# Performance work log

Measured on AMD Instinct MI355X. Metric: run time of the kernel, lower is better.

## Reference

```python
import jax, jax.numpy as jnp
import numpy as np

BS, S, D, H, HS, HSEL, L = 32, 512, 512, 8, 2, 4, 6
DK = D // H  # 64
HD = H - HS  # dynamic heads


def setup_inputs() -> dict:
    key = jax.random.key(0)
    ks = jax.random.split(key, 10)
    w = lambda k, shape: jax.random.normal(k, shape, dtype=jnp.float32) * 0.02
    return {
        'q_embed_data': jax.random.normal(ks[0], (BS, S, D), jnp.float32),
        'qa_embed_data': jax.random.normal(ks[1], (BS, S, D), jnp.float32),
        # stacked per-layer params (torch Linear convention: W[out,in], y = x@W.T+b)
        'Wq': w(ks[2], (L, D, D)), 'bq': jnp.zeros((L, D), jnp.float32),
        'Wv': w(ks[3], (L, D, D)), 'bv': jnp.zeros((L, D), jnp.float32),
        'Wg': w(ks[4], (L, HD, D)),                      # routing gate, no bias
        'Wo': w(ks[5], (L, D, D)), 'bo': jnp.zeros((L, D), jnp.float32),
        'ln1_g': jnp.ones((L, D), jnp.float32), 'ln1_b': jnp.zeros((L, D), jnp.float32),
        'W1': w(ks[6], (L, D, D)), 'b1': jnp.zeros((L, D), jnp.float32),
        'W2': w(ks[7], (L, D, D)), 'b2': jnp.zeros((L, D), jnp.float32),
        'ln2_g': jnp.ones((L, D), jnp.float32), 'ln2_b': jnp.zeros((L, D), jnp.float32),
    }


def _layer_norm(x, g, b):
    m = x.mean(-1, keepdims=True)
    v = ((x - m) ** 2).mean(-1, keepdims=True)
    return (x - m) * jax.lax.rsqrt(v + 1e-5) * g + b


def _moh_attention(xq, xv, Wq, bq, Wv, bv, Wg, Wo, bo, strict):
    bs, s, d = xq.shape
    q = xq @ Wq.T + bq            # kq_same=True: k = q projection
    v = xv @ Wv.T + bv
    qh = q.reshape(bs, s, H, DK).transpose(0, 2, 1, 3)   # [b,h,s,dk]
    vh = v.reshape(bs, s, H, DK).transpose(0, 2, 1, 3)
    scores = jnp.einsum('bhqd,bhkd->bhqk', qh, qh) / jnp.sqrt(jnp.float32(DK))
    # mask==1 -> causal incl. diag; mask==0 -> strictly causal
    allow = jnp.tril(jnp.ones((s, s), bool), k=-1 if strict else 0)
    scores = jnp.where(allow, scores, jnp.float32(-1e9))
    # pad-zero shift: first query row replaced by zeros -> uniform attention
    scores = scores.at[:, :, 0, :].set(0.0)
    # per-token top-k head routing over dynamic heads
    gates = jax.nn.softmax(q.reshape(bs * s, D) @ Wg.T, axis=-1)  # [bs*s, HD]
    _, idx = jax.lax.top_k(gates, HSEL)
    dmask = jnp.zeros_like(gates).at[jnp.arange(bs * s)[:, None], idx].set(1.0)
    dyn = (gates * dmask).reshape(bs, s, HD)
    routing = jnp.concatenate([jnp.ones((bs, s, HS), gates.dtype), dyn], -1).mean(1)  # [b,H]
    attn = jax.nn.softmax(scores, axis=-1)
    ctx = jnp.einsum('bhqk,bhkd->bhqd', attn, vh) * routing[:, :, None, None]
    out = ctx.transpose(0, 2, 1, 3).reshape(bs, s, D) @ Wo.T + bo
    f = dmask.sum(0)
    P = gates.mean(0)
    balance = jnp.sum((f / (f.sum() + 1e-5)) * (P / (P.sum() + 1e-5)))
    return out, balance


def reference(q_embed_data, qa_embed_data, Wq, bq, Wv, bv, Wg, Wo, bo,
              ln1_g, ln1_b, W1, b1, W2, b2, ln2_g, ln2_b):
    def layer(i, xq, xv, strict):
        a, bl = _moh_attention(xq, xv, Wq[i], bq[i], Wv[i], bv[i], Wg[i], Wo[i], bo[i], strict)
        x = _layer_norm(xq + a, ln1_g[i], ln1_b[i])
        ffn = jax.nn.relu(x @ W1[i].T + b1[i]) @ W2[i].T + b2[i]
        return _layer_norm(x + ffn, ln2_g[i], ln2_b[i]), bl

    y = qa_embed_data
    x = q_embed_data
    # blocks_1: self-attention on y, mask=1
    y, _ = layer(0, y, y, False)
    y, _ = layer(1, y, y, False)
    # blocks_2: alternate mask=1 self-attn / mask=0 cross-attn (values=y)
    x, _ = layer(2, x, x, False)
    x, bl = layer(3, x, y, True)
    x, _ = layer(4, x, x, False)
    x, bl = layer(5, x, y, True)
    return (x, bl)
```

## Files before the change

kernel.cpp:

```cpp
#include <hip/hip_runtime.h>
#include <cstdint>

#define BSZ 32
#define SEQ 512
#define DM  512
#define NH  8
#define DK  64
#define HS_ 2
#define HD_ 6
#define NL  6
#define MROWS (BSZ*SEQ)
#define QVLD 1024
#define SCL 0.18033688011112043f

typedef unsigned short bf16_t;
typedef __attribute__((ext_vector_type(4))) float f32x4;
typedef __attribute__((ext_vector_type(8))) short bf16x8;
typedef __attribute__((ext_vector_type(8))) unsigned short u16x8;

#define DEV static __device__ __forceinline__

DEV float bf2f(bf16_t b) {
  unsigned int u = ((unsigned int)b) << 16;
  float f; __builtin_memcpy(&f, &u, 4); return f;
}
DEV bf16_t f2b(float f) {
  unsigned int u; __builtin_memcpy(&u, &f, 4);
  unsigned int r = (u + 0x7fffu + ((u >> 16) & 1u)) >> 16;
  return (bf16_t)r;
}
DEV void unp2(unsigned int w, float& a, float& b) {
  unsigned int ua = w << 16, ub = w & 0xffff0000u;
  __builtin_memcpy(&a, &ua, 4); __builtin_memcpy(&b, &ub, 4);
}
DEV unsigned cvtpk(float lo, float hi) {
  unsigned r;
  asm("v_cvt_pk_bf16_f32 %0, %1, %2" : "=v"(r) : "v"(lo), "v"(hi));
  return r;
}

DEV void gload_lds16(const bf16_t* g, bf16_t* l) {
  __builtin_amdgcn_global_load_lds(
      (const __attribute__((address_space(1))) void*)g,
      (__attribute__((address_space(3))) void*)l, 16, 0, 0);
}

DEV bf16x8 scale_q(bf16x8 v) {
  u16x8 u;
  __builtin_memcpy(&u, &v, 16);
  unsigned w[4];
#pragma unroll
  for (int e = 0; e < 4; ++e)
    w[e] = cvtpk(bf2f(u[2 * e]) * SCL, bf2f(u[2 * e + 1]) * SCL);
  bf16x8 r;
  __builtin_memcpy(&r, w, 16);
  return r;
}

__global__ __launch_bounds__(256) void f2b2_kernel(
    const float* __restrict__ s0, const float* __restrict__ s1,
    bf16_t* __restrict__ d0, bf16_t* __restrict__ d1) {
  const float* s = blockIdx.y ? s1 : s0;
  bf16_t* d = blockIdx.y ? d1 : d0;
  const int i = blockIdx.x * 256 + threadIdx.x;
  float4 v = reinterpret_cast<const float4*>(s)[i];
  ushort4 o;
  o.x = f2b(v.x); o.y = f2b(v.y); o.z = f2b(v.z); o.w = f2b(v.w);
  reinterpret_cast<ushort4*>(d)[i] = o;
}

__global__ __launch_bounds__(256) void f2bw_kernel(
    const float* __restrict__ s0, const float* __restrict__ s1,
    const float* __restrict__ s2, const float* __restrict__ s3,
    const float* __restrict__ s4, bf16_t* __restrict__ dst) {
  const float* srcs[5] = {s0, s1, s2, s3, s4};
  const float* s = srcs[blockIdx.y];
  bf16_t* d = dst + (size_t)blockIdx.y * ((size_t)NL * DM * DM);
  const int i = blockIdx.x * 256 + threadIdx.x;
  float4 v = reinterpret_cast<const float4*>(s)[i];
  ushort4 o;
  o.x = f2b(v.x); o.y = f2b(v.y); o.z = f2b(v.z); o.w = f2b(v.w);
  reinterpret_cast<ushort4*>(d)[i] = o;
}

template <int NB, int NWG, bool RELU>
__global__ __launch_bounds__(512) void gemm8(
    const bf16_t* __restrict__ A0, const bf16_t* __restrict__ A1,
    const bf16_t* __restrict__ W0, const bf16_t* __restrict__ W1,
    const float* __restrict__ b0, const float* __restrict__ b1,
    bf16_t* __restrict__ Yb, int ldy) {
  const int K = 512;
  const int lin = blockIdx.y * NB + blockIdx.x;
  const int cpx = NWG / 8;
  const int swz = (lin & 7) * cpx + (lin >> 3);
  const int bn = swz % NB, bm = swz / NB;
  const int tid = threadIdx.x, wid = tid >> 6, lane = tid & 63;
  const int wr = wid >> 2, wc = wid & 3;
  const int lrow = lane & 15, grp = lane >> 4;
  const int l3 = lane >> 3, c3 = lane & 7;

  __shared__ __align__(16) bf16_t Lds[3][24576];

  const bool hi = (bn * 256) >= 512;
  const bf16_t* Asel = hi ? A1 : A0;
  const bf16_t* Wsel = hi ? (W1 - (size_t)512 * K) : W0;
  const float* bsel = hi ? (b1 - 512) : b0;

  f32x4 acc[4][4];
#pragma unroll
  for (int m = 0; m < 4; ++m)
#pragma unroll
    for (int n = 0; n < 4; ++n) acc[m][n] = f32x4{0.f, 0.f, 0.f, 0.f};

  const char* LB = (const char*)Lds;

  auto stage3 = [&](int kt, int buf, int half) {
#pragma unroll
    for (int cc = 0; cc < 3; ++cc) {
      const int c = wid + (half * 3 + cc) * 8;
      const int colb = ((c3 ^ l3) * 8);
      if (c < 16) {
        gload_lds16(Asel + (size_t)(bm * 128 + c * 8 + l3) * K + kt * 64 + colb,
                    &Lds[buf][c * 512]);
      } else {
        const int cb = c - 16;
        gload_lds16(Wsel + (size_t)(bn * 256 + cb * 8 + l3) * K + kt * 64 + colb,
                    &Lds[buf][8192 + cb * 512]);
      }
    }
  };
  auto rdA = [&](int buf, int rA, int ks) -> bf16x8 {
    const int off = buf * 49152 + rA * 128 + ((ks * 64 + grp * 16) ^ ((rA & 7) << 4));
    return *reinterpret_cast<const bf16x8*>(LB + off);
  };
  auto rdB = [&](int buf, int rB, int ks) -> bf16x8 {
    const int off = buf * 49152 + 16384 + rB * 128 + ((ks * 64 + grp * 16) ^ ((rB & 7) << 4));
    return *reinterpret_cast<const bf16x8*>(LB + off);
  };

  stage3(0, 0, 0); stage3(0, 0, 1);
  stage3(1, 1, 0); stage3(1, 1, 1);
  asm volatile("s_waitcnt vmcnt(6)" ::: "memory");
  __builtin_amdgcn_s_barrier();

  for (int g = 0; g < 8; ++g) {
    const int bufR = g % 3, bufW = (g + 2) % 3;
    const bool st = g < 6;
    bf16x8 bwv[4][2], afv[2][2];
#pragma unroll
    for (int n = 0; n < 4; ++n)
#pragma unroll
      for (int ks = 0; ks < 2; ++ks)
        bwv[n][ks] = rdB(bufR, wc * 64 + n * 16 + lrow, ks);
#pragma unroll
    for (int m = 0; m < 2; ++m)
#pragma unroll
      for (int ks = 0; ks < 2; ++ks)
        afv[m][ks] = rdA(bufR, wr * 64 + m * 16 + lrow, ks);
    if (st) stage3(g + 2, bufW, 0);
    __builtin_amdgcn_s_barrier();
    asm volatile("s_waitcnt lgkmcnt(0)" ::: "memory");
    __builtin_amdgcn_s_setprio(1);
#pragma unroll
    for (int ks = 0; ks < 2; ++ks)
#pragma unroll
      for (int m = 0; m < 2; ++m)
#pragma unroll
        for (int n = 0; n < 4; ++n)
          acc[m][n] = __builtin_amdgcn_mfma_f32_16x16x32_bf16(afv[m][ks], bwv[n][ks], acc[m][n], 0, 0, 0);
    __builtin_amdgcn_s_setprio(0);
    __builtin_amdgcn_s_barrier();
#pragma unroll
    for (int m = 0; m < 2; ++m)
#pragma unroll
      for (int ks = 0; ks < 2; ++ks)
        afv[m][ks] = rdA(bufR, wr * 64 + 32 + m * 16 + lrow, ks);
    if (st) stage3(g + 2, bufW, 1);
    __builtin_amdgcn_s_barrier();
    asm volatile("s_waitcnt lgkmcnt(0)" ::: "memory");
    __builtin_amdgcn_s_setprio(1);
#pragma unroll
    for (int ks = 0; ks < 2; ++ks)
#pragma unroll
      for (int m = 0; m < 2; ++m)
#pragma unroll
        for (int n = 0; n < 4; ++n)
          acc[2 + m][n] = __builtin_amdgcn_mfma_f32_16x16x32_bf16(afv[m][ks], bwv[n][ks], acc[2 + m][n], 0, 0, 0);
    __builtin_amdgcn_s_setprio(0);
    if (g < 6) {
      asm volatile("s_waitcnt vmcnt(6)" ::: "memory");
    } else if (g == 6) {
      asm volatile("s_waitcnt vmcnt(0)" ::: "memory");
    }
    __builtin_amdgcn_s_barrier();
  }

  const int r0 = bm * 128 + wr * 64 + grp * 4;
  const int c0 = bn * 256 + wc * 64 + lrow;
#pragma unroll
  for (int n = 0; n < 4; ++n) {
    const int col = c0 + n * 16;
    const float bc = bsel[col];
#pragma unroll
    for (int qm = 0; qm < 4; ++qm)
#pragma unroll
      for (int j = 0; j < 4; ++j) {
        float v = acc[qm][n][j] + bc;
        if (RELU) v = fmaxf(v, 0.f);
        Yb[(size_t)(r0 + qm * 16 + j) * ldy + col] = f2b(v);
      }
  }
}

template <int OUT>
__global__ __launch_bounds__(512) void gemm_ln(
    const bf16_t* __restrict__ A, const bf16_t* __restrict__ W,
    const float* __restrict__ bias, const bf16_t* __restrict__ Res,
    const float* __restrict__ gam, const float* __restrict__ bet,
    bf16_t* __restrict__ outb, float* __restrict__ outf) {
  const int K = 512;
  const int bm = blockIdx.x;
  const int tid = threadIdx.x, wid = tid >> 6, lane = tid & 63;
  const int lrow = lane & 15, grp = lane >> 4;
  const int l3 = lane >> 3, c3 = lane & 7;

  __shared__ __align__(16) bf16_t Lds[2][36864];
  __shared__ float red_s[64][8], red_q[64][8], stat[64][2];

  f32x4 acc[4][4];
#pragma unroll
  for (int m = 0; m < 4; ++m)
#pragma unroll
    for (int n = 0; n < 4; ++n) acc[m][n] = f32x4{0.f, 0.f, 0.f, 0.f};

  const char* LB = (const char*)Lds;

  auto stage = [&](int kt, int buf) {
#pragma unroll
    for (int k = 0; k < 9; ++k) {
      const int c = wid + k * 8;
      const int colb = (c3 ^ l3) * 8;
      if (c < 8) {
        gload_lds16(A + (size_t)(bm * 64 + c * 8 + l3) * K + kt * 64 + colb,
                    &Lds[buf][c * 512]);
      } else {
        const int cb = c - 8;
        gload_lds16(W + (size_t)(cb * 8 + l3) * K + kt * 64 + colb,
                    &Lds[buf][4096 + cb * 512]);
      }
    }
  };
  auto rdA = [&](int buf, int r, int ks) -> bf16x8 {
    const int off = buf * 73728 + r * 128 + ((ks * 64 + grp * 16) ^ ((r & 7) << 4));
    return *reinterpret_cast<const bf16x8*>(LB + off);
  };
  auto rdW = [&](int buf, int r, int ks) -> bf16x8 {
    const int off = buf * 73728 + 8192 + r * 128 + ((ks * 64 + grp * 16) ^ ((r & 7) << 4));
    return *reinterpret_cast<const bf16x8*>(LB + off);
  };

  stage(0, 0);
  __syncthreads();
  for (int g = 0; g < 8; ++g) {
    const int bufR = g & 1;
    if (g < 7) stage(g + 1, bufR ^ 1);
    bf16x8 af[4][2], wf[4][2];
#pragma unroll
    for (int m = 0; m < 4; ++m)
#pragma unroll
      for (int ks = 0; ks < 2; ++ks)
        af[m][ks] = rdA(bufR, m * 16 + lrow, ks);
#pragma unroll
    for (int n = 0; n < 4; ++n)
#pragma unroll
      for (int ks = 0; ks < 2; ++ks)
        wf[n][ks] = rdW(bufR, wid * 64 + n * 16 + lrow, ks);
    __builtin_amdgcn_s_setprio(1);
#pragma unroll
    for (int ks = 0; ks < 2; ++ks)
#pragma unroll
      for (int m = 0; m < 4; ++m)
#pragma unroll
        for (int n = 0; n < 4; ++n)
          acc[m][n] = __builtin_amdgcn_mfma_f32_16x16x32_bf16(af[m][ks], wf[n][ks], acc[m][n], 0, 0, 0);
    __builtin_amdgcn_s_setprio(0);
    __syncthreads();
  }

  const int cbase = wid * 64;
  float bias_n[4], gam_n[4], bet_n[4];
#pragma unroll
  for (int n = 0; n < 4; ++n) {
    bias_n[n] = bias[cbase + n * 16 + lrow];
    gam_n[n]  = gam[cbase + n * 16 + lrow];
    bet_n[n]  = bet[cbase + n * 16 + lrow];
  }
  const size_t rowg0 = (size_t)bm * 64;
  float ps[4][4], pq[4][4];
#pragma unroll
  for (int m = 0; m < 4; ++m)
#pragma unroll
    for (int j = 0; j < 4; ++j) {
      const int r = m * 16 + grp * 4 + j;
      float s = 0.f, q = 0.f;
#pragma unroll
      for (int n = 0; n < 4; ++n) {
        float z = acc[m][n][j] + bias_n[n] +
                  bf2f(Res[(rowg0 + r) * DM + cbase + n * 16 + lrow]);
        acc[m][n][j] = z;
        s += z; q += z * z;
      }
      ps[m][j] = s; pq[m][j] = q;
    }
#pragma unroll
  for (int m = 0; m < 4; ++m)
#pragma unroll
    for (int j = 0; j < 4; ++j)
#pragma unroll
      for (int off = 1; off <= 8; off <<= 1) {
        ps[m][j] += __shfl_xor(ps[m][j], off);
        pq[m][j] += __shfl_xor(pq[m][j], off);
      }
  if (lrow == 0) {
#pragma unroll
    for (int m = 0; m < 4; ++m)
#pragma unroll
      for (int j = 0; j < 4; ++j) {
        const int r = m * 16 + grp * 4 + j;
        red_s[r][wid] = ps[m][j];
        red_q[r][wid] = pq[m][j];
      }
  }
  __syncthreads();
  if (tid < 64) {
    float s = 0.f, q = 0.f;
#pragma unroll
    for (int w = 0; w < 8; ++w) { s += red_s[tid][w]; q += red_q[tid][w]; }
    const float mean = s * (1.f / 512.f);
    const float var = q * (1.f / 512.f) - mean * mean;
    stat[tid][0] = mean;
    stat[tid][1] = rsqrtf(var + 1e-5f);
  }
  __syncthreads();
#pragma unroll
  for (int m = 0; m < 4; ++m)
#pragma unroll
    for (int j = 0; j < 4; ++j) {
      const int r = m * 16 + grp * 4 + j;
      const float mean = stat[r][0], rstd = stat[r][1];
#pragma unroll
      for (int n = 0; n < 4; ++n) {
        const float o = (acc[m][n][j] - mean) * rstd * gam_n[n] + bet_n[n];
        const size_t off = (rowg0 + r) * DM + cbase + n * 16 + lrow;
        if (OUT == 0) outb[off] = f2b(o);
        else outf[off] = o;
      }
    }
}

__global__ __launch_bounds__(256) void gates_kernel(
    const bf16_t* __restrict__ qv, const float* __restrict__ Wg,
    float* __restrict__ rdyn, float* __restrict__ fP) {
  __shared__ float wg_s[HD_ * DM];
  __shared__ float blk[4][18];
  const int tid = threadIdx.x, wid = tid >> 6, lane = tid & 63;
  for (int i = tid; i < HD_ * DM / 4; i += 256)
    reinterpret_cast<float4*>(wg_s)[i] = reinterpret_cast<const float4*>(Wg)[i];
  __syncthreads();
  const int bb = blockIdx.x >> 4;
  const int t0 = (blockIdx.x & 15) * 32 + wid * 8;
  float fs[6] = {0, 0, 0, 0, 0, 0}, ps[6] = {0, 0, 0, 0, 0, 0}, rs[6] = {0, 0, 0, 0, 0, 0};
  for (int it = 0; it < 8; ++it) {
    const int tok = bb * SEQ + t0 + it;
    uint4 u = reinterpret_cast<const uint4*>(qv + (size_t)tok * QVLD)[lane];
    float x[8];
    unp2(u.x, x[0], x[1]); unp2(u.y, x[2], x[3]);
    unp2(u.z, x[4], x[5]); unp2(u.w, x[6], x[7]);
    float g[6];
#pragma unroll
    for (int j = 0; j < 6; ++j) {
      float p = 0.f;
#pragma unroll
      for (int e = 0; e < 8; ++e) p = fmaf(x[e], wg_s[j * DM + lane * 8 + e], p);
#pragma unroll
      for (int off = 32; off; off >>= 1) p += __shfl_xor(p, off);
      g[j] = p;
    }
    float mx = g[0];
#pragma unroll
    for (int j = 1; j < 6; ++j) mx = fmaxf(mx, g[j]);
    float se = 0.f;
#pragma unroll
    for (int j = 0; j < 6; ++j) { g[j] = __expf(g[j] - mx); se += g[j]; }
    float inv = 1.f / se;
#pragma unroll
    for (int j = 0; j < 6; ++j) g[j] *= inv;
    int d1 = 0;
#pragma unroll
    for (int j = 1; j < 6; ++j)
      if (g[j] < g[d1] || (g[j] == g[d1] && j > d1)) d1 = j;
    int d2 = (d1 == 0) ? 1 : 0;
#pragma unroll
    for (int j = 0; j < 6; ++j) {
      if (j == d1) continue;
      if (g[j] < g[d2] || (g[j] == g[d2] && j > d2)) d2 = j;
    }
#pragma unroll
    for (int j = 0; j < 6; ++j) {
      const bool drop = (j == d1) || (j == d2);
      fs[j] += drop ? 0.f : 1.f;
      ps[j] += g[j];
      rs[j] += drop ? 0.f : g[j];
    }
  }
  if (lane == 0) {
#pragma unroll
    for (int j = 0; j < 6; ++j) {
      blk[wid][j] = fs[j]; blk[wid][6 + j] = ps[j]; blk[wid][12 + j] = rs[j];
    }
  }
  __syncthreads();
  if (tid < 18) {
    float s = blk[0][tid] + blk[1][tid] + blk[2][tid] + blk[3][tid];
    if (tid < 12) atomicAdd(&fP[tid], s);
    else atomicAdd(&rdyn[bb * 6 + (tid - 12)], s * (1.f / 512.f));
  }
}

__global__ __launch_bounds__(256, 4) void fattn_kernel(
    const bf16_t* __restrict__ qv, const float* __restrict__ rdyn,
    bf16_t* __restrict__ ctx, int strict) {
  const int bh = blockIdx.x, qt = blockIdx.y;
  const int b = bh >> 3, h = bh & 7;
  const int tid = threadIdx.x, wid = tid >> 6, lane = tid & 63;
  const int c0 = lane & 15, grp = lane >> 4;
  const int l3 = lane >> 3, c3 = lane & 7;
  const int kidx = lane & 31, dhalf = lane >> 5;

  __shared__ __align__(16) bf16_t Ks[64 * 64];
  __shared__ __align__(16) bf16_t Vt[64 * 72];
  __shared__ __align__(16) bf16_t Ps[4][32 * 64];
  __shared__ float csum[64];

  const bf16_t* qp = qv;
  const bf16_t* vp = qv + 512;
  const float factor = (h < HS_) ? 1.f : rdyn[b * 6 + (h - HS_)];

  const int qbase = qt * 128 + wid * 32;

  bf16x8 qf[2][2];
#pragma unroll
  for (int nt = 0; nt < 2; ++nt)
#pragma unroll
    for (int ks = 0; ks < 2; ++ks)
      qf[nt][ks] = scale_q(*reinterpret_cast<const bf16x8*>(
          qp + ((size_t)(b * SEQ + qbase + nt * 16 + c0)) * QVLD + h * DK + ks * 32 + grp * 8));

  f32x4 acc[2][4];
#pragma unroll
  for (int m = 0; m < 2; ++m)
#pragma unroll
    for (int d = 0; d < 4; ++d) acc[m][d] = f32x4{0.f, 0.f, 0.f, 0.f};
  float mreg[2] = {-3e38f, -3e38f};
  float lreg[2] = {0.f, 0.f};
  float cs[8] = {0, 0, 0, 0, 0, 0, 0, 0};

  const int lastk = (qbase + 31 - strict) >> 6;
  const int ktmax = 2 * qt + 1;

  for (int kt = 0; kt <= ktmax; ++kt) {
#pragma unroll
    for (int i = 0; i < 2; ++i) {
      int row = i * 32 + wid * 8 + l3;
      int blk = c3 ^ l3;
      gload_lds16(qp + ((size_t)(b * SEQ + kt * 64 + row)) * QVLD + h * DK + blk * 8,
                  Ks + (i * 32 + wid * 8) * 64);
    }
#pragma unroll
    for (int j = 0; j < 2; ++j) {
      const int d0 = (wid * 2 + j) * 8 + dhalf * 4;
      const bf16_t* src = vp + ((size_t)(b * SEQ + kt * 64 + 2 * kidx)) * QVLD + h * DK + d0;
      ushort4 lo = *reinterpret_cast<const ushort4*>(src);
      ushort4 hv = *reinterpret_cast<const ushort4*>(src + QVLD);
      *reinterpret_cast<unsigned*>(&Vt[(d0 + 0) * 72 + 2 * kidx]) = (unsigned)lo.x | ((unsigned)hv.x << 16);
      *reinterpret_cast<unsigned*>(&Vt[(d0 + 1) * 72 + 2 * kidx]) = (unsigned)lo.y | ((unsigned)hv.y << 16);
      *reinterpret_cast<unsigned*>(&Vt[(d0 + 2) * 72 + 2 * kidx]) = (unsigned)lo.z | ((unsigned)hv.z << 16);
      *reinterpret_cast<unsigned*>(&Vt[(d0 + 3) * 72 + 2 * kidx]) = (unsigned)lo.w | ((unsigned)hv.w << 16);
      if (qt == 3) {
        cs[j * 4 + 0] += bf2f(lo.x) + bf2f(hv.x);
        cs[j * 4 + 1] += bf2f(lo.y) + bf2f(hv.y);
        cs[j * 4 + 2] += bf2f(lo.z) + bf2f(hv.z);
        cs[j * 4 + 3] += bf2f(lo.w) + bf2f(hv.w);
      }
    }
    __syncthreads();

    if (kt <= lastk) {
      const char* KsB = (const char*)Ks;
      bf16x8 kf[4][2];
#pragma unroll
      for (int mt = 0; mt < 4; ++mt)
#pragma unroll
        for (int ks = 0; ks < 2; ++ks)
          kf[mt][ks] = *reinterpret_cast<const bf16x8*>(
              KsB + (mt * 16 + c0) * 128 + 16 * ((4 * ks + grp) ^ (c0 & 7)));
      f32x4 s[4][2];
#pragma unroll
      for (int mt = 0; mt < 4; ++mt)
#pragma unroll
        for (int nt = 0; nt < 2; ++nt) s[mt][nt] = f32x4{0.f, 0.f, 0.f, 0.f};
      __builtin_amdgcn_s_setprio(1);
#pragma unroll
      for (int mt = 0; mt < 4; ++mt)
#pragma unroll
        for (int nt = 0; nt < 2; ++nt)
#pragma unroll
          for (int ks = 0; ks < 2; ++ks)
            s[mt][nt] = __builtin_amdgcn_mfma_f32_16x16x32_bf16(
                kf[mt][ks], qf[nt][ks], s[mt][nt], 0, 0, 0);
      __builtin_amdgcn_s_setprio(0);

      const bool masked = (kt == lastk);
      if (masked) {
#pragma unroll
        for (int nt = 0; nt < 2; ++nt) {
          const int q = qbase + nt * 16 + c0;
#pragma unroll
          for (int mt = 0; mt < 4; ++mt)
#pragma unroll
            for (int j = 0; j < 4; ++j) {
              int k = kt * 64 + mt * 16 + grp * 4 + j;
              if (k + strict > q) s[mt][nt][j] = -1e30f;
            }
        }
      }
      float mx[2];
#pragma unroll
      for (int nt = 0; nt < 2; ++nt) {
        float a = fmaxf(s[0][nt][0], s[0][nt][1]);
        a = fmaxf(fmaxf(a, s[0][nt][2]), s[0][nt][3]);
        float bm_ = fmaxf(s[1][nt][0], s[1][nt][1]);
        bm_ = fmaxf(fmaxf(bm_, s[1][nt][2]), s[1][nt][3]);
        float c = fmaxf(s[2][nt][0], s[2][nt][1]);
        c = fmaxf(fmaxf(c, s[2][nt][2]), s[2][nt][3]);
        float d = fmaxf(s[3][nt][0], s[3][nt][1]);
        d = fmaxf(fmaxf(d, s[3][nt][2]), s[3][nt][3]);
        float m_ = fmaxf(fmaxf(a, bm_), fmaxf(c, d));
        m_ = fmaxf(m_, __shfl_xor(m_, 16));
        m_ = fmaxf(m_, __shfl_xor(m_, 32));
        mx[nt] = m_;
      }
      const bool defer = __all((mx[0] - mreg[0] <= 8.f) && (mx[1] - mreg[1] <= 8.f));
      float sc[2];
#pragma unroll
      for (int nt = 0; nt < 2; ++nt) {
        const float mnew = defer ? mreg[nt] : fmaxf(mreg[nt], mx[nt]);
        float ts = 0.f;
#pragma unroll
        for (int mt = 0; mt < 4; ++mt)
#pragma unroll
          for (int j = 0; j < 4; ++j) {
            float pp = exp2f(s[mt][nt][j] - mnew);
            s[mt][nt][j] = pp; ts += pp;
          }
        ts += __shfl_xor(ts, 16);
        ts += __shfl_xor(ts, 32);
        if (defer) {
          lreg[nt] += ts;
        } else {
          sc[nt] = exp2f(mreg[nt] - mnew);
          lreg[nt] = lreg[nt] * sc[nt] + ts;
          mreg[nt] = mnew;
        }
      }
      char* PsB = (char*)(&Ps[wid][0]);
#pragma unroll
      for (int nt = 0; nt < 2; ++nt)
#pragma unroll
        for (int mt = 0; mt < 4; ++mt) {
          uint2 w;
          w.x = cvtpk(s[mt][nt][0], s[mt][nt][1]);
          w.y = cvtpk(s[mt][nt][2], s[mt][nt][3]);
          int row = nt * 16 + c0;
          int off = (row * 128 + mt * 32 + grp * 8) ^ ((c0 & 7) << 4);
          *reinterpret_cast<uint2*>(PsB + off) = w;
        }
      if (!defer) {
#pragma unroll
        for (int mtq = 0; mtq < 2; ++mtq) {
          f32x4 sv;
#pragma unroll
          for (int j = 0; j < 4; ++j) sv[j] = __shfl(sc[mtq], grp * 4 + j);
#pragma unroll
          for (int dt = 0; dt < 4; ++dt) acc[mtq][dt] *= sv;
        }
      }
      bf16x8 pf[2][2], vf2[4][2];
#pragma unroll
      for (int mtq = 0; mtq < 2; ++mtq)
#pragma unroll
        for (int ks = 0; ks < 2; ++ks)
          pf[mtq][ks] = *reinterpret_cast<const bf16x8*>(
              PsB + (mtq * 16 + c0) * 128 + 16 * ((4 * ks + grp) ^ (c0 & 7)));
#pragma unroll
      for (int dt = 0; dt < 4; ++dt)
#pragma unroll
        for (int ks = 0; ks < 2; ++ks)
          vf2[dt][ks] = *reinterpret_cast<const bf16x8*>(
              (const char*)Vt + (dt * 16 + c0) * 144 + ks * 64 + grp * 16);
      __builtin_amdgcn_s_setprio(1);
#pragma unroll
      for (int mtq = 0; mtq < 2; ++mtq)
#pragma unroll
        for (int dt = 0; dt < 4; ++dt)
#pragma unroll
          for (int ks = 0; ks < 2; ++ks)
            acc[mtq][dt] = __builtin_amdgcn_mfma_f32_16x16x32_bf16(
                pf[mtq][ks], vf2[dt][ks], acc[mtq][dt], 0, 0, 0);
      __builtin_amdgcn_s_setprio(0);
    }
    __syncthreads();
  }

  if (qt == 3) {
#pragma unroll
    for (int e = 0; e < 8; ++e)
#pragma unroll
      for (int off = 1; off <= 16; off <<= 1) cs[e] += __shfl_xor(cs[e], off);
    if ((lane & 31) == 0) {
#pragma unroll
      for (int e = 0; e < 8; ++e)
        csum[(wid * 2 + (e >> 2)) * 8 + dhalf * 4 + (e & 3)] = cs[e];
    }
    __syncthreads();
    if (tid < 64)
      ctx[((size_t)(b * SEQ)) * DM + h * DK + tid] = f2b(csum[tid] * (1.f / 512.f) * factor);
  }

#pragma unroll
  for (int mtq = 0; mtq < 2; ++mtq) {
    const float inv = factor / lreg[mtq];
    f32x4 iv;
#pragma unroll
    for (int j = 0; j < 4; ++j) iv[j] = __shfl(inv, grp * 4 + j);
#pragma unroll
    for (int j = 0; j < 4; ++j) {
      const int q = qbase + mtq * 16 + grp * 4 + j;
      if (q == 0) continue;
#pragma unroll
      for (int dt = 0; dt < 4; ++dt)
        ctx[((size_t)(b * SEQ + q)) * DM + h * DK + dt * 16 + c0] =
            f2b(acc[mtq][dt][j] * iv[j]);
    }
  }
}

__global__ void balance_kernel(const float* __restrict__ fP, float* __restrict__ out) {
  if (threadIdx.x == 0 && blockIdx.x == 0) {
    float fs = 0.f, pssum = 0.f, P[6];
    for (int j = 0; j < 6; ++j) {
      fs += fP[j];
      P[j] = fP[6 + j] * (1.f / (float)MROWS);
      pssum += P[j];
    }
    float bal = 0.f;
    for (int j = 0; j < 6; ++j)
      bal += (fP[j] / (fs + 1e-5f)) * (P[j] / (pssum + 1e-5f));
    out[0] = bal;
  }
}

extern "C" void kernel_launch(void* const* d_in, const int* in_sizes, int n_in,
                              void* d_out, int out_size, void* d_ws, size_t ws_size,
                              hipStream_t stream) {
  (void)in_sizes; (void)n_in; (void)out_size; (void)ws_size;
  const float* q_embed  = (const float*)d_in[0];
  const float* qa_embed = (const float*)d_in[1];
  const float* Wq  = (const float*)d_in[2];
  const float* bq  = (const float*)d_in[3];
  const float* Wv  = (const float*)d_in[4];
  const float* bv  = (const float*)d_in[5];
  const float* Wg  = (const float*)d_in[6];
  const float* Wo  = (const float*)d_in[7];
  const float* bo  = (const float*)d_in[8];
  const float* ln1g = (const float*)d_in[9];
  const float* ln1b = (const float*)d_in[10];
  const float* W1  = (const float*)d_in[11];
  const float* b1  = (const float*)d_in[12];
  const float* W2  = (const float*)d_in[13];
  const float* b2  = (const float*)d_in[14];
  const float* ln2g = (const float*)d_in[15];
  const float* ln2b = (const float*)d_in[16];

  char* p = (char*)d_ws;
  auto alloc = [&](size_t bytes) -> char* {
    char* r = p; p += (bytes + 255) & ~(size_t)255; return r;
  };
  const size_t WDE = (size_t)NL * DM * DM;
  const size_t AE  = (size_t)MROWS * DM;
  bf16_t* wall_b = (bf16_t*)alloc(5 * WDE * 2);
  bf16_t* wq_b = wall_b;
  bf16_t* wv_b = wall_b + WDE;
  bf16_t* wo_b = wall_b + 2 * WDE;
  bf16_t* w1_b = wall_b + 3 * WDE;
  bf16_t* w2_b = wall_b + 4 * WDE;
  bf16_t* y_b   = (bf16_t*)alloc(AE * 2);
  bf16_t* x_b   = (bf16_t*)alloc(AE * 2);
  bf16_t* qv_b  = (bf16_t*)alloc((size_t)MROWS * QVLD * 2);
  bf16_t* ctx_b = (bf16_t*)alloc(AE * 2);
  bf16_t* x1_b  = (bf16_t*)alloc(AE * 2);
  bf16_t* ffn1_b = (bf16_t*)alloc(AE * 2);
  float* stats = (float*)alloc(NL * (12 + BSZ * 6) * 4);
  float* fPbase = stats;
  float* rdynbase = stats + NL * 12;

  hipMemsetAsync(stats, 0, NL * (12 + BSZ * 6) * 4, stream);

  f2bw_kernel<<<dim3((unsigned)(WDE / 4 / 256), 5), 256, 0, stream>>>(
      Wq, Wv, Wo, W1, W2, wall_b);
  f2b2_kernel<<<dim3((unsigned)(AE / 4 / 256), 2), 256, 0, stream>>>(
      qa_embed, q_embed, y_b, x_b);

  const size_t DD = (size_t)DM * DM;
  dim3 gqv(4, 128), gn5(2, 128), gfa(256, 4), gln(256);
  float* outx = (float*)d_out;

  auto layer = [&](int i, bf16_t* resb, const bf16_t* xvb, int strict, bool last) {
    float* fP = fPbase + i * 12;
    float* rdyn = rdynbase + i * (BSZ * 6);
    gemm8<4, 512, false><<<gqv, 512, 0, stream>>>(
        resb, xvb, wq_b + i * DD, wv_b + i * DD, bq + i * DM, bv + i * DM, qv_b, QVLD);
    gates_kernel<<<MROWS / 32, 256, 0, stream>>>(qv_b, Wg + (size_t)i * HD_ * DM, rdyn, fP);
    fattn_kernel<<<gfa, 256, 0, stream>>>(qv_b, rdyn, ctx_b, strict);
    gemm_ln<0><<<gln, 512, 0, stream>>>(
        ctx_b, wo_b + i * DD, bo + i * DM, resb, ln1g + i * DM, ln1b + i * DM,
        x1_b, nullptr);
    gemm8<2, 256, true><<<gn5, 512, 0, stream>>>(
        x1_b, x1_b, w1_b + i * DD, w1_b + i * DD, b1 + i * DM, b1 + i * DM, ffn1_b, DM);
    if (last)
      gemm_ln<1><<<gln, 512, 0, stream>>>(
          ffn1_b, w2_b + i * DD, b2 + i * DM, x1_b, ln2g + i * DM, ln2b + i * DM,
          nullptr, outx);
    else
      gemm_ln<0><<<gln, 512, 0, stream>>>(
          ffn1_b, w2_b + i * DD, b2 + i * DM, x1_b, ln2g + i * DM, ln2b + i * DM,
          resb, nullptr);
  };

  layer(0, y_b, y_b, 0, false);
  layer(1, y_b, y_b, 0, false);
  layer(2, x_b, x_b, 0, false);
  layer(3, x_b, y_b, 1, false);
  layer(4, x_b, x_b, 0, false);
  layer(5, x_b, y_b, 1, true);
  balance_kernel<<<1, 64, 0, stream>>>(fPbase + 5 * 12, outx + (size_t)MROWS * DM);
}
```

Before: 951.5 us.

## Batch independent layers 0 and 2 into shared grid launches

Layers 0 (on y) and 2 (on x) do not depend on each other, so they now run together: each kernel takes two argument structs and uses a grid z or y dimension to pick one. This doubles the grid size for that unit and removes six kernel launches, aiming to fill the GPU better and overlap the two independent chains. Separate qv, ctx, x1 and ffn1 buffers are allocated for the second stream. The fattn launch bound also changes from 4 to 2 blocks per SM, which relaxes register pressure but may lower occupancy.

```diff
diff --git a/kernel.cpp b/kernel.cpp
--- a/kernel.cpp
+++ b/kernel.cpp
@@ -56,6 +56,12 @@
   __builtin_memcpy(&r, w, 16);
   return r;
 }
+
+struct G8A { const bf16_t *A0, *A1, *W0, *W1; const float *b0, *b1; bf16_t* Y; };
+struct GLA { const bf16_t *A, *W; const float* bias; const bf16_t* Res;
+             const float *gam, *bet; bf16_t* outb; float* outf; };
+struct FAA { const bf16_t* qv; const float* rdyn; bf16_t* ctx; };
+struct GTA { const bf16_t* qv; const float* Wg; float* rdyn; float* fP; };
 
 __global__ __launch_bounds__(256) void f2b2_kernel(
     const float* __restrict__ s0, const float* __restrict__ s1,
@@ -84,11 +90,8 @@
 }
 
 template <int NB, int NWG, bool RELU>
-__global__ __launch_bounds__(512) void gemm8(
-    const bf16_t* __restrict__ A0, const bf16_t* __restrict__ A1,
-    const bf16_t* __restrict__ W0, const bf16_t* __restrict__ W1,
-    const float* __restrict__ b0, const float* __restrict__ b1,
-    bf16_t* __restrict__ Yb, int ldy) {
+__global__ __launch_bounds__(512) void gemm8(G8A ia, G8A ib, int ldy) {
+  const G8A& P = blockIdx.z ? ib : ia;
   const int K = 512;
   const int lin = blockIdx.y * NB + blockIdx.x;
   const int cpx = NWG / 8;
@@ -102,9 +105,9 @@
   __shared__ __align__(16) bf16_t Lds[3][24576];
 
   const bool hi = (bn * 256) >= 512;
-  const bf16_t* Asel = hi ? A1 : A0;
-  const bf16_t* Wsel = hi ? (W1 - (size_t)512 * K) : W0;
-  const float* bsel = hi ? (b1 - 512) : b0;
+  const bf16_t* Asel = hi ? P.A1 : P.A0;
+  const bf16_t* Wsel = hi ? (P.W1 - (size_t)512 * K) : P.W0;
+  const float* bsel = hi ? (P.b1 - 512) : P.b0;
 
   f32x4 acc[4][4];
 #pragma unroll
@@ -207,17 +210,14 @@
       for (int j = 0; j < 4; ++j) {
         float v = acc[qm][n][j] + bc;
         if (RELU) v = fmaxf(v, 0.f);
-        Yb[(size_t)(r0 + qm * 16 + j) * ldy + col] = f2b(v);
+        P.Y[(size_t)(r0 + qm * 16 + j) * ldy + col] = f2b(v);
       }
   }
 }
 
 template <int OUT>
-__global__ __launch_bounds__(512) void gemm_ln(
-    const bf16_t* __restrict__ A, const bf16_t* __restrict__ W,
-    const float* __restrict__ bias, const bf16_t* __restrict__ Res,
-    const float* __restrict__ gam, const float* __restrict__ bet,
-    bf16_t* __restrict__ outb, float* __restrict__ outf) {
+__global__ __launch_bounds__(512) void gemm_ln(GLA ia, GLA ib) {
+  const GLA& P = blockIdx.y ? ib : ia;
   const int K = 512;
   const int bm = blockIdx.x;
   const int tid = threadIdx.x, wid = tid >> 6, lane = tid & 63;
@@ -241,11 +241,11 @@
       const int c = wid + k * 8;
       const int colb = (c3 ^ l3) * 8;
       if (c < 8) {
-        gload_lds16(A + (size_t)(bm * 64 + c * 8 + l3) * K + kt * 64 + colb,
+        gload_lds16(P.A + (size_t)(bm * 64 + c * 8 + l3) * K + kt * 64 + colb,
                     &Lds[buf][c * 512]);
       } else {
         const int cb = c - 8;
-        gload_lds16(W + (size_t)(cb * 8 + l3) * K + kt * 64 + colb,
+        gload_lds16(P.W + (size_t)(cb * 8 + l3) * K + kt * 64 + colb,
                     &Lds[buf][4096 + cb * 512]);
       }
     }
@@ -291,9 +291,9 @@
   float bias_n[4], gam_n[4], bet_n[4];
 #pragma unroll
   for (int n = 0; n < 4; ++n) {
-    bias_n[n] = bias[cbase + n * 16 + lrow];
-    gam_n[n]  = gam[cbase + n * 16 + lrow];
-    bet_n[n]  = bet[cbase + n * 16 + lrow];
+    bias_n[n] = P.bias[cbase + n * 16 + lrow];
+    gam_n[n]  = P.gam[cbase + n * 16 + lrow];
+    bet_n[n]  = P.bet[cbase + n * 16 + lrow];
   }
   const size_t rowg0 = (size_t)bm * 64;
   float ps[4][4], pq[4][4];
@@ -306,7 +306,7 @@
 #pragma unroll
       for (int n = 0; n < 4; ++n) {
         float z = acc[m][n][j] + bias_n[n] +
-                  bf2f(Res[(rowg0 + r) * DM + cbase + n * 16 + lrow]);
+                  bf2f(P.Res[(rowg0 + r) * DM + cbase + n * 16 + lrow]);
         acc[m][n][j] = z;
         s += z; q += z * z;
       }
@@ -352,27 +352,26 @@
       for (int n = 0; n < 4; ++n) {
         const float o = (acc[m][n][j] - mean) * rstd * gam_n[n] + bet_n[n];
         const size_t off = (rowg0 + r) * DM + cbase + n * 16 + lrow;
-        if (OUT == 0) outb[off] = f2b(o);
-        else outf[off] = o;
-      }
-    }
-}
-
-__global__ __launch_bounds__(256) void gates_kernel(
-    const bf16_t* __restrict__ qv, const float* __restrict__ Wg,
-    float* __restrict__ rdyn, float* __restrict__ fP) {
+        if (OUT == 0) P.outb[off] = f2b(o);
+        else P.outf[off] = o;
+      }
+    }
+}
+
+__global__ __launch_bounds__(256) void gates_kernel(GTA ia, GTA ib) {
+  const GTA& P = blockIdx.y ? ib : ia;
   __shared__ float wg_s[HD_ * DM];
   __shared__ float blk[4][18];
   const int tid = threadIdx.x, wid = tid >> 6, lane = tid & 63;
   for (int i = tid; i < HD_ * DM / 4; i += 256)
-    reinterpret_cast<float4*>(wg_s)[i] = reinterpret_cast<const float4*>(Wg)[i];
+    reinterpret_cast<float4*>(wg_s)[i] = reinterpret_cast<const float4*>(P.Wg)[i];
   __syncthreads();
   const int bb = blockIdx.x >> 4;
   const int t0 = (blockIdx.x & 15) * 32 + wid * 8;
   float fs[6] = {0, 0, 0, 0, 0, 0}, ps[6] = {0, 0, 0, 0, 0, 0}, rs[6] = {0, 0, 0, 0, 0, 0};
   for (int it = 0; it < 8; ++it) {
     const int tok = bb * SEQ + t0 + it;
-    uint4 u = reinterpret_cast<const uint4*>(qv + (size_t)tok * QVLD)[lane];
+    uint4 u = reinterpret_cast<const uint4*>(P.qv + (size_t)tok * QVLD)[lane];
     float x[8];
     unp2(u.x, x[0], x[1]); unp2(u.y, x[2], x[3]);
     unp2(u.z, x[4], x[5]); unp2(u.w, x[6], x[7]);
@@ -422,14 +421,13 @@
   __syncthreads();
   if (tid < 18) {
     float s = blk[0][tid] + blk[1][tid] + blk[2][tid] + blk[3][tid];
-    if (tid < 12) atomicAdd(&fP[tid], s);
-    else atomicAdd(&rdyn[bb * 6 + (tid - 12)], s * (1.f / 512.f));
-  }
-}
-
-__global__ __launch_bounds__(256, 4) void fattn_kernel(
-    const bf16_t* __restrict__ qv, const float* __restrict__ rdyn,
-    bf16_t* __restrict__ ctx, int strict) {
+    if (tid < 12) atomicAdd(&P.fP[tid], s);
+    else atomicAdd(&P.rdyn[bb * 6 + (tid - 12)], s * (1.f / 512.f));
+  }
+}
+
+__global__ __launch_bounds__(256, 2) void fattn_kernel(FAA ia, FAA ib, int strict) {
+  const FAA& P = blockIdx.z ? ib : ia;
   const int bh = blockIdx.x, qt = blockIdx.y;
   const int b = bh >> 3, h = bh & 7;
   const int tid = threadIdx.x, wid = tid >> 6, lane = tid & 63;
@@ -442,9 +440,9 @@
   __shared__ __align__(16) bf16_t Ps[4][32 * 64];
   __shared__ float csum[64];
 
-  const bf16_t* qp = qv;
-  const bf16_t* vp = qv + 512;
-  const float factor = (h < HS_) ? 1.f : rdyn[b * 6 + (h - HS_)];
+  const bf16_t* qp = P.qv;
+  const bf16_t* vp = P.qv + 512;
+  const float factor = (h < HS_) ? 1.f : P.rdyn[b * 6 + (h - HS_)];
 
   const int qbase = qt * 128 + wid * 32;
 
@@ -634,7 +632,7 @@
     }
     __syncthreads();
     if (tid < 64)
-      ctx[((size_t)(b * SEQ)) * DM + h * DK + tid] = f2b(csum[tid] * (1.f / 512.f) * factor);
+      P.ctx[((size_t)(b * SEQ)) * DM + h * DK + tid] = f2b(csum[tid] * (1.f / 512.f) * factor);
   }
 
 #pragma unroll
@@ -649,7 +647,7 @@
       if (q == 0) continue;
 #pragma unroll
       for (int dt = 0; dt < 4; ++dt)
-        ctx[((size_t)(b * SEQ + q)) * DM + h * DK + dt * 16 + c0] =
+        P.ctx[((size_t)(b * SEQ + q)) * DM + h * DK + dt * 16 + c0] =
             f2b(acc[mtq][dt][j] * iv[j]);
     }
   }
@@ -707,9 +705,13 @@
   bf16_t* y_b   = (bf16_t*)alloc(AE * 2);
   bf16_t* x_b   = (bf16_t*)alloc(AE * 2);
   bf16_t* qv_b  = (bf16_t*)alloc((size_t)MROWS * QVLD * 2);
-  bf16_t* ctx_b = (bf16_t*)alloc(AE * 2);
-  bf16_t* x1_b  = (bf16_t*)alloc(AE * 2);
-  bf16_t* ffn1_b = (bf16_t*)alloc(AE * 2);
+  bf16_t* qv2_b = (bf16_t*)alloc((size_t)MROWS * QVLD * 2);
+  bf16_t* ctx_b  = (bf16_t*)alloc(AE * 2);
+  bf16_t* ctx2_b = (bf16_t*)alloc(AE * 2);
+  bf16_t* x1_b   = (bf16_t*)alloc(AE * 2);
+  bf16_t* x12_b  = (bf16_t*)alloc(AE * 2);
+  bf16_t* ffn1_b  = (bf16_t*)alloc(AE * 2);
+  bf16_t* ffn12_b = (bf16_t*)alloc(AE * 2);
   float* stats = (float*)alloc(NL * (12 + BSZ * 6) * 4);
   float* fPbase = stats;
   float* rdynbase = stats + NL * 12;
@@ -722,36 +724,48 @@
       qa_embed, q_embed, y_b, x_b);
 
   const size_t DD = (size_t)DM * DM;
-  dim3 gqv(4, 128), gn5(2, 128), gfa(256, 4), gln(256);
   float* outx = (float*)d_out;
 
-  auto layer = [&](int i, bf16_t* resb, const bf16_t* xvb, int strict, bool last) {
-    float* fP = fPbase + i * 12;
-    float* rdyn = rdynbase + i * (BSZ * 6);
-    gemm8<4, 512, false><<<gqv, 512, 0, stream>>>(
-        resb, xvb, wq_b + i * DD, wv_b + i * DD, bq + i * DM, bv + i * DM, qv_b, QVLD);
-    gates_kernel<<<MROWS / 32, 256, 0, stream>>>(qv_b, Wg + (size_t)i * HD_ * DM, rdyn, fP);
-    fattn_kernel<<<gfa, 256, 0, stream>>>(qv_b, rdyn, ctx_b, strict);
-    gemm_ln<0><<<gln, 512, 0, stream>>>(
-        ctx_b, wo_b + i * DD, bo + i * DM, resb, ln1g + i * DM, ln1b + i * DM,
-        x1_b, nullptr);
-    gemm8<2, 256, true><<<gn5, 512, 0, stream>>>(
-        x1_b, x1_b, w1_b + i * DD, w1_b + i * DD, b1 + i * DM, b1 + i * DM, ffn1_b, DM);
-    if (last)
-      gemm_ln<1><<<gln, 512, 0, stream>>>(
-          ffn1_b, w2_b + i * DD, b2 + i * DM, x1_b, ln2g + i * DM, ln2b + i * DM,
-          nullptr, outx);
-    else
-      gemm_ln<0><<<gln, 512, 0, stream>>>(
-          ffn1_b, w2_b + i * DD, b2 + i * DM, x1_b, ln2g + i * DM, ln2b + i * DM,
-          resb, nullptr);
+  struct Bufs { bf16_t *qv, *ctx, *x1, *ffn1; };
+  Bufs B0{qv_b, ctx_b, x1_b, ffn1_b}, B1{qv2_b, ctx2_b, x12_b, ffn12_b};
+
+  auto unit = [&](int nb, int i0, int i1, bf16_t* res0, const bf16_t* xv0,
+                  bf16_t* res1, const bf16_t* xv1, int strict, bool last) {
+    G8A qa{res0, xv0, wq_b + i0 * DD, wv_b + i0 * DD, bq + i0 * DM, bv + i0 * DM, B0.qv};
+    G8A qb{res1, xv1, wq_b + i1 * DD, wv_b + i1 * DD, bq + i1 * DM, bv + i1 * DM, B1.qv};
+    gemm8<4, 512, false><<<dim3(4, 128, nb), 512, 0, stream>>>(qa, qb, QVLD);
+
+    GTA ga{B0.qv, Wg + (size_t)i0 * HD_ * DM, rdynbase + i0 * (BSZ * 6), fPbase + i0 * 12};
+    GTA gb{B1.qv, Wg + (size_t)i1 * HD_ * DM, rdynbase + i1 * (BSZ * 6), fPbase + i1 * 12};
+    gates_kernel<<<dim3(MROWS / 32, nb), 256, 0, stream>>>(ga, gb);
+
+    FAA fa{B0.qv, rdynbase + i0 * (BSZ * 6), B0.ctx};
+    FAA fb{B1.qv, rdynbase + i1 * (BSZ * 6), B1.ctx};
+    fattn_kernel<<<dim3(256, 4, nb), 256, 0, stream>>>(fa, fb, strict);
+
+    GLA la{B0.ctx, wo_b + i0 * DD, bo + i0 * DM, res0, ln1g + i0 * DM, ln1b + i0 * DM, B0.x1, nullptr};
+    GLA lb{B1.ctx, wo_b + i1 * DD, bo + i1 * DM, res1, ln1g + i1 * DM, ln1b + i1 * DM, B1.x1, nullptr};
+    gemm_ln<0><<<dim3(256, nb), 512, 0, stream>>>(la, lb);
+
+    G8A f1a{B0.x1, B0.x1, w1_b + i0 * DD, w1_b + i0 * DD, b1 + i0 * DM, b1 + i0 * DM, B0.ffn1};
+    G8A f1b{B1.x1, B1.x1, w1_b + i1 * DD, w1_b + i1 * DD, b1 + i1 * DM, b1 + i1 * DM, B1.ffn1};
+    gemm8<2, 256, true><<<dim3(2, 128, nb), 512, 0, stream>>>(f1a, f1b, DM);
+
+    GLA m0{B0.ffn1, w2_b + i0 * DD, b2 + i0 * DM, B0.x1, ln2g + i0 * DM, ln2b + i0 * DM, res0, nullptr};
+    GLA m1{B1.ffn1, w2_b + i1 * DD, b2 + i1 * DM, B1.x1, ln2g + i1 * DM, ln2b + i1 * DM, res1, nullptr};
+    if (last) {
+      m0.outb = nullptr; m0.outf = outx;
+      gemm_ln<1><<<dim3(256, nb), 512, 0, stream>>>(m0, m1);
+    } else {
+      gemm_ln<0><<<dim3(256, nb), 512, 0, stream>>>(m0, m1);
+    }
   };
 
-  layer(0, y_b, y_b, 0, false);
-  layer(1, y_b, y_b, 0, false);
-  layer(2, x_b, x_b, 0, false);
-  layer(3, x_b, y_b, 1, false);
-  layer(4, x_b, x_b, 0, false);
-  layer(5, x_b, y_b, 1, true);
+  unit(2, 0, 2, y_b, y_b, x_b, x_b, 0, false);
+  unit(1, 1, 1, y_b, y_b, y_b, y_b, 0, false);
+  unit(1, 3, 3, x_b, y_b, x_b, y_b, 1, false);
+  unit(1, 4, 4, x_b, x_b, x_b, x_b, 0, false);
+  unit(1, 5, 5, x_b, y_b, x_b, y_b, 1, true);
+
   balance_kernel<<<1, 64, 0, stream>>>(fPbase + 5 * 12, outx + (size_t)MROWS * DM);
 }
```

New measurement: 894.9 us. 5.9% less time.
